# Kernel tuning notes

Measured on AMD Instinct MI355X. Metric: run time of the kernel, lower is better.

The kernel has to match this reference:

```python
import jax, jax.numpy as jnp
import numpy as np
import math

NUM_HEAD = 8
QK_DIM = 32       # in_dim // num_head
V_DIM = 32
KV_STRIDE = 2
Q_STRIDE = 1
LOCAL_RANGE = 16  # hard_range
POS_DIM = 256     # position_embedding_dim (= in_dim)
POS_MAG = 1.0
WAVE = 1000.0


def _position_feats(h, w, h_kv, w_kv, fcx_w, fcy_w):
    # sinusoidal embedding of (query_pos - key_pos), then linear projection per head
    fr = jnp.arange(POS_DIM // 4, dtype=jnp.float32)
    dim_mat = WAVE ** (4.0 / POS_DIM * fr)                 # (POS_DIM/4,)

    def emb(n_q, n_kv):
        diff = (jnp.arange(n_q, dtype=jnp.float32)[:, None] * Q_STRIDE
                - jnp.arange(n_kv, dtype=jnp.float32)[None, :] * KV_STRIDE) * POS_MAG
        a = diff[:, :, None] / dim_mat                      # (n_q, n_kv, POS_DIM/4)
        return jnp.concatenate([jnp.sin(a), jnp.cos(a)], axis=2)  # (n_q, n_kv, POS_DIM/2)

    inv_sqrt2 = 1.0 / math.sqrt(2.0)
    pfx = jnp.einsum('wkf,of->wko', emb(w, w_kv), fcx_w)
    pfx = pfx.reshape(w, w_kv, NUM_HEAD, QK_DIM).transpose(2, 0, 1, 3) * inv_sqrt2  # (H,w,w_kv,d)
    pfy = jnp.einsum('ykf,of->yko', emb(h, h_kv), fcy_w)
    pfy = pfy.reshape(h, h_kv, NUM_HEAD, QK_DIM).transpose(2, 0, 1, 3) * inv_sqrt2  # (H,h,h_kv,d)
    return pfx, pfy


def _local_mask(h, w, h_kv, w_kv):
    # True where attention is FORBIDDEN (matches masked_fill_ semantics of the map)
    R, s = LOCAL_RANGE, KV_STRIDE

    def axis_keep(n_q, n_kv):
        i = jnp.arange(n_q)
        k = jnp.arange(n_kv)
        lo = jnp.maximum((i - R) // s, 0)
        hi = (i + R + 1) // s + 1
        return (k[None, :] >= lo[:, None]) & (k[None, :] < hi[:, None])  # (n_q, n_kv)

    keep_y = axis_keep(h, h_kv)
    keep_x = axis_keep(w, w_kv)
    keep = keep_y[:, None, :, None] & keep_x[None, :, None, :]  # (h,w,h_kv,w_kv)
    return ~keep


def reference(x_input, q_w, k_w, v_w, fcx_w, fcy_w, appr_bias, geom_bias,
              proj_w, proj_b, gamma):
    n, c, h, w = x_input.shape
    H, d = NUM_HEAD, QK_DIM
    x_q = x_input                                   # q_stride == 1
    x_kv = x_input[:, :, ::KV_STRIDE, ::KV_STRIDE]  # AvgPool(kernel=1, stride=2)
    h_kv, w_kv = x_kv.shape[2], x_kv.shape[3]

    # 1x1 conv projections
    q = jnp.einsum('nchw,oc->nohw', x_q, q_w).reshape(n, H, d, h, w).transpose(0, 1, 3, 4, 2)  # (n,H,h,w,d)
    k = jnp.einsum('nchw,oc->nohw', x_kv, k_w).reshape(n, H, d, h_kv * w_kv)                   # (n,H,d,K)
    v = jnp.einsum('nchw,oc->nohw', x_kv, v_w).reshape(n, H, V_DIM, h_kv * w_kv).transpose(0, 1, 3, 2)  # (n,H,K,v)

    pfx, pfy = _position_feats(h, w, h_kv, w_kv, fcx_w, fcy_w)
    ab = appr_bias.reshape(1, H, 1, 1, d)
    gb = geom_bias.reshape(1, H, 1, 1, d)

    # appr-appr + bias-appr:  (q + appr_bias) @ k
    energy = jnp.einsum('nhyxd,nhdk->nhyxk', q + ab, k).reshape(n, H, h, w, h_kv, w_kv)
    # appr-position + bias-position, separable over x and y
    qg = q + gb
    energy = energy + jnp.einsum('nhyxd,hxkd->nhyxk', qg, pfx)[:, :, :, :, None, :]
    energy = energy + jnp.einsum('nhyxd,hykd->nhyxk', qg, pfy)[:, :, :, :, :, None]

    mask = _local_mask(h, w, h_kv, w_kv)  # (h,w,h_kv,w_kv), True = masked
    energy = jnp.where(mask[None, None], -jnp.inf, energy)
    energy = energy.reshape(n, H, h * w, h_kv * w_kv)

    attn = jax.nn.softmax(energy, axis=3)
    out = jnp.einsum('nhqk,nhkv->nhqv', attn, v)               # (n,H,h*w,v)
    out = out.transpose(0, 1, 3, 2).reshape(n, H * V_DIM, h, w)
    out = jnp.einsum('nchw,oc->nohw', out, proj_w) + proj_b[None, :, None, None]
    return gamma.reshape(()) * out + x_input


def setup_inputs() -> dict:
    key = jax.random.key(0)
    ks = jax.random.split(key, 11)
    s = 0.05  # keep attention logits in a sane range
    return {
        'x_input': jax.random.normal(ks[0], (2, 256, 64, 64), jnp.float32),
        'q_w': jax.random.normal(ks[1], (256, 256), jnp.float32) * s,
        'k_w': jax.random.normal(ks[2], (256, 256), jnp.float32) * s,
        'v_w': jax.random.normal(ks[3], (256, 256), jnp.float32) * s,
        'fcx_w': jax.random.normal(ks[4], (256, 128), jnp.float32) * s,
        'fcy_w': jax.random.normal(ks[5], (256, 128), jnp.float32) * s,
        'appr_bias': jax.random.normal(ks[6], (256,), jnp.float32) * s,
        'geom_bias': jax.random.normal(ks[7], (256,), jnp.float32) * s,
        'proj_w': jax.random.normal(ks[8], (256, 256), jnp.float32) * s,
        'proj_b': jax.random.normal(ks[9], (256,), jnp.float32) * s,
        'gamma': jax.random.normal(ks[10], (1,), jnp.float32),
    }
```

## Files before the change

### kernel.cpp

```cpp
#include <hip/hip_runtime.h>
#include <hip/hip_bf16.h>
#include <math.h>

#define NB   2
#define CC   256
#define PQ   4096
#define PKV  1024

#define NF (-INFINITY)
#define M0 24.0f
#define EXSTRIDE 36
#define EYSTRIDE 20

typedef __attribute__((ext_vector_type(8))) short short8;
typedef __attribute__((ext_vector_type(4))) float f32x4;

__global__ __launch_bounds__(256) void prep_kernel(
    const float* __restrict__ q_w, const float* __restrict__ k_w,
    const float* __restrict__ v_w, const float* __restrict__ proj_w,
    __hip_bfloat16* __restrict__ qw_b, __hip_bfloat16* __restrict__ kw_b,
    __hip_bfloat16* __restrict__ vw_b, __hip_bfloat16* __restrict__ pw_b,
    const float* __restrict__ fcx, const float* __restrict__ fcy,
    __hip_bfloat16* __restrict__ pembx_b, __hip_bfloat16* __restrict__ pemby_b,
    const float* __restrict__ x, __hip_bfloat16* __restrict__ xb) {
  __shared__ __align__(16) float shbuf[64 * 65];
  const int bid = blockIdx.x;
  const int tid = threadIdx.x;
  if (bid < 256) {
    const int which = bid >> 6;
    const float* src = (which == 0) ? q_w : (which == 1) ? k_w
                       : (which == 2) ? v_w : proj_w;
    __hip_bfloat16* dst = (which == 0) ? qw_b : (which == 1) ? kw_b
                          : (which == 2) ? vw_b : pw_b;
    const int i = (bid & 63) * 256 + tid;
    const float4 v = reinterpret_cast<const float4*>(src)[i];
    short4 s;
    s.x = __builtin_bit_cast(short, __float2bfloat16(v.x));
    s.y = __builtin_bit_cast(short, __float2bfloat16(v.y));
    s.z = __builtin_bit_cast(short, __float2bfloat16(v.z));
    s.w = __builtin_bit_cast(short, __float2bfloat16(v.w));
    reinterpret_cast<short4*>(dst)[i] = s;
  } else if (bid < 508) {
    float* feat = shbuf;
    const int pb = bid - 256;
    const int dd = pb >> 1;
    const int which = pb & 1;
    const float* FC = which ? fcy : fcx;
    __hip_bfloat16* OUT = which ? pemby_b : pembx_b;
    if (tid < 64) {
      const float diff = (float)(dd - 62);
      const float dm = powf(1000.f, (float)tid * (1.f / 64.f));
      const float aa = diff / dm;
      feat[tid] = sinf(aa);
      feat[tid + 64] = cosf(aa);
    }
    __syncthreads();
    const float4* row4 = reinterpret_cast<const float4*>(FC + tid * 128);
    const float4* f4 = reinterpret_cast<const float4*>(feat);
    float s0 = 0.f, s1 = 0.f, s2 = 0.f, s3 = 0.f;
#pragma unroll
    for (int f = 0; f < 32; ++f) {
      const float4 fv = f4[f];
      const float4 rv = row4[f];
      s0 = fmaf(fv.x, rv.x, s0);
      s1 = fmaf(fv.y, rv.y, s1);
      s2 = fmaf(fv.z, rv.z, s2);
      s3 = fmaf(fv.w, rv.w, s3);
    }
    const float s = ((s0 + s1) + (s2 + s3)) * 0.70710678118654752440f;
    OUT[(size_t)dd * 256 + tid] = __float2bfloat16(s);
  } else {
    float (*t)[65] = reinterpret_cast<float(*)[65]>(shbuf);
    const int b = bid - 508;
    const int p0 = (b & 63) * 64;
    const int c0 = ((b >> 6) & 3) * 64;
    const int n = b >> 8;
    {
      const int pl = tid & 63, cg = tid >> 6;
#pragma unroll
      for (int i = 0; i < 16; ++i) {
        const int cl = cg * 16 + i;
        t[cl][pl] = x[((size_t)n * 256 + c0 + cl) * PQ + p0 + pl];
      }
    }
    __syncthreads();
    const int cl = tid & 63;
#pragma unroll
    for (int j = 0; j < 16; ++j) {
      const int pl = (tid >> 6) + 4 * j;
      ((__hip_bfloat16*)xb)[((size_t)n * PQ + p0 + pl) * 256 + c0 + cl] =
          __float2bfloat16(t[cl][pl]);
    }
  }
}

__global__ __launch_bounds__(256) void gemm_qkv_kernel(
    const __hip_bfloat16* __restrict__ xb,
    const __hip_bfloat16* __restrict__ qw, const __hip_bfloat16* __restrict__ kw,
    const __hip_bfloat16* __restrict__ vw, const float* __restrict__ ab,
    const float* __restrict__ gb, __hip_bfloat16* __restrict__ qab,
    __hip_bfloat16* __restrict__ qgb, __hip_bfloat16* __restrict__ k_lb,
    __hip_bfloat16* __restrict__ v_t) {
  const int bid = blockIdx.x;
  const int tid = threadIdx.x;
  const int wv = tid >> 6, l = tid & 63, lc = l & 15, lq = l >> 4;
  if (bid < 1024) {
    const int n = bid & 1;
    const int o0 = ((bid >> 1) & 3) * 64;
    const int p0 = (bid >> 3) * 32;
    const short* ar =
        (const short*)qw + ((size_t)(o0 + wv * 16 + lc)) * 256 + 8 * lq;
    const short* bbase =
        (const short*)xb + ((size_t)n * PQ + p0) * 256 + 8 * lq;
    const short* b0p = bbase + (size_t)(0 + lc) * 256;
    const short* b1p = bbase + (size_t)(16 + lc) * 256;
    f32x4 acc0 = {0.f, 0.f, 0.f, 0.f};
    f32x4 acc1 = {0.f, 0.f, 0.f, 0.f};
#pragma unroll
    for (int kt = 0; kt < 8; ++kt) {
      const short8 af = *reinterpret_cast<const short8*>(ar + kt * 32);
      acc0 = __builtin_amdgcn_mfma_f32_16x16x32_bf16(
          af, *reinterpret_cast<const short8*>(b0p + kt * 32), acc0, 0, 0, 0);
      acc1 = __builtin_amdgcn_mfma_f32_16x16x32_bf16(
          af, *reinterpret_cast<const short8*>(b1p + kt * 32), acc1, 0, 0, 0);
    }
#pragma unroll
    for (int r = 0; r < 4; ++r) {
      const int o = o0 + wv * 16 + 4 * lq + r;
      const float abo = ab[o], gbo = gb[o];
      const int head = o >> 5, dd = o & 31;
      const size_t gbase = (size_t)(n * 8 + head) * PQ;
      const float a_[2] = {acc0[r], acc1[r]};
#pragma unroll
      for (int nf = 0; nf < 2; ++nf) {
        const int p = p0 + 16 * nf + lc;
        const size_t idx = (gbase + p) * 32 + dd;
        qab[idx] = __float2bfloat16(a_[nf] + abo);
        qgb[idx] = __float2bfloat16(a_[nf] + gbo);
      }
    }
  } else {
    const int kb2 = bid - 1024;
    const int n = kb2 & 1;
    const int o0 = ((kb2 >> 1) & 3) * 64;
    const bool isV = ((kb2 >> 3) & 1) != 0;
    const int p0 = (kb2 >> 4) * 32;
    const __hip_bfloat16* W = isV ? vw : kw;
    const short* ar =
        (const short*)W + ((size_t)(o0 + wv * 16 + lc)) * 256 + 8 * lq;
    const short* bb = (const short*)xb + (size_t)n * PQ * 256 + 8 * lq;
    const int pk0 = p0 + 0 + lc, pk1 = p0 + 16 + lc;
    const short* b0p = bb + (size_t)((pk0 >> 5) * 128 + (pk0 & 31) * 2) * 256;
    const short* b1p = bb + (size_t)((pk1 >> 5) * 128 + (pk1 & 31) * 2) * 256;
    f32x4 acc0 = {0.f, 0.f, 0.f, 0.f};
    f32x4 acc1 = {0.f, 0.f, 0.f, 0.f};
#pragma unroll
    for (int kt = 0; kt < 8; ++kt) {
      const short8 af = *reinterpret_cast<const short8*>(ar + kt * 32);
      acc0 = __builtin_amdgcn_mfma_f32_16x16x32_bf16(
          af, *reinterpret_cast<const short8*>(b0p + kt * 32), acc0, 0, 0, 0);
      acc1 = __builtin_amdgcn_mfma_f32_16x16x32_bf16(
          af, *reinterpret_cast<const short8*>(b1p + kt * 32), acc1, 0, 0, 0);
    }
#pragma unroll
    for (int r = 0; r < 4; ++r) {
      const int o = o0 + wv * 16 + 4 * lq + r;
      const int head = o >> 5, dd = o & 31;
      const float a_[2] = {acc0[r], acc1[r]};
#pragma unroll
      for (int nf = 0; nf < 2; ++nf) {
        const int p = p0 + 16 * nf + lc;
        if (!isV) {
          k_lb[((size_t)(n * 8 + head) * PKV + p) * 32 + dd] =
              __float2bfloat16(a_[nf]);
        } else {
          v_t[((size_t)(n * 8 + head) * 32 + dd) * PKV + p] =
              __float2bfloat16(a_[nf]);
        }
      }
    }
  }
}

__global__ __launch_bounds__(256) void exy_kernel(
    const __hip_bfloat16* __restrict__ qgb_b,
    const __hip_bfloat16* __restrict__ pembx_b,
    const __hip_bfloat16* __restrict__ pemby_b, float* __restrict__ EX,
    float* __restrict__ EY) {
  const int MODE = blockIdx.z;
  const int i = blockIdx.x;
  const int g = blockIdx.y;
  const int head = g & 7;
  const __hip_bfloat16* pemb_b = MODE ? pemby_b : pembx_b;
  const int wv = threadIdx.x >> 6;
  const int l = threadIdx.x & 63;
  const int lc = l & 15, lq = l >> 4;

  const int rowi = wv * 16 + lc;
  const int p = (MODE == 0) ? rowi * 64 + i : i * 64 + rowi;
  const short8 a = *reinterpret_cast<const short8*>(
      (const short*)qgb_b + ((size_t)g * PQ + p) * 32 + 8 * lq);

  int drow0, drow1;
  if (MODE == 0) {
    drow0 = i - 2 * lc + 62;
    drow1 = i - 2 * (lc + 16) + 62;
  } else {
    const int lo_y = max((i - 16) >> 1, 0);
    drow0 = i - 2 * (lo_y + lc) + 62;
    drow1 = i - 2 * (lo_y + lc + 16) + 62;
  }
  const short8 b0 = *reinterpret_cast<const short8*>(
      (const short*)pemb_b + (size_t)drow0 * 256 + head * 32 + 8 * lq);
  const short8 b1 = *reinterpret_cast<const short8*>(
      (const short*)pemb_b + (size_t)drow1 * 256 + head * 32 + 8 * lq);

  const f32x4 zero = {0.f, 0.f, 0.f, 0.f};
  const f32x4 c0 = __builtin_amdgcn_mfma_f32_16x16x32_bf16(a, b0, zero, 0, 0, 0);
  const f32x4 c1 = __builtin_amdgcn_mfma_f32_16x16x32_bf16(a, b1, zero, 0, 0, 0);

#pragma unroll
  for (int r = 0; r < 4; ++r) {
    const int rowr = wv * 16 + 4 * lq + r;
    const int pr = (MODE == 0) ? rowr * 64 + i : i * 64 + rowr;
    if (MODE == 0) {
      const int lox = max((i - 16) >> 1, 0);
      const int hix = min(((i + 17) >> 1) + 1, 32);
      float* o = EX + ((size_t)g * PQ + pr) * EXSTRIDE;
      o[lc] = (lc >= lox && lc < hix) ? (c0[r] - M0) : -1e30f;
      o[16 + lc] = (lc + 16 >= lox && lc + 16 < hix) ? (c1[r] - M0) : -1e30f;
      if (lc < 4) o[32 + lc] = -1e30f;
    } else {
      float* o = EY + ((size_t)g * PQ + pr) * EYSTRIDE;
      o[lc] = c0[r];
      if (lc < 4) o[16 + lc] = c1[r];
    }
  }
}

__global__ __launch_bounds__(512, 8) void attn_mfma_kernel(
    const __hip_bfloat16* __restrict__ qab_b,
    const __hip_bfloat16* __restrict__ k_lb,
    const __hip_bfloat16* __restrict__ v_t, const float* __restrict__ EX,
    const float* __restrict__ EY, __hip_bfloat16* __restrict__ attb) {
  const int g = blockIdx.y;
  const int nImg = g >> 3, hd = g & 7;
  const int bx = blockIdx.x & 3;
  const int by = blockIdx.x >> 2;
  const int tx = bx * 16;
  const int wv = threadIdx.x >> 6;
  const int yw = wv & 3;
  const int s = wv >> 2;
  const int y = by * 4 + yw;
  const int l = threadIdx.x & 63;
  const int lc = l & 15;
  const int lq = l >> 4;

  __shared__ float eybuf[4][EYSTRIDE][16];
  __shared__ float mrg[4][64][9];
  __shared__ float obuf[4][16][33];

  const int KLO = max((tx - 16) >> 1, 0);
  const int lo_y = max((y - 16) >> 1, 0);
  const int hi_y = min(((y + 17) >> 1) + 1, 32);
  const int NKY = hi_y - lo_y;

  const int xq = tx + lc;
  const int pq_ = y * 64 + xq;

  const short8 qa = *reinterpret_cast<const short8*>(
      (const short*)qab_b + ((size_t)g * PQ + pq_) * 32 + 8 * lq);

  const float* exr = EX + ((size_t)g * PQ + pq_) * EXSTRIDE;
  float exC0[4], exC1[4];
#pragma unroll
  for (int r = 0; r < 4; ++r) {
    exC0[r] = exr[KLO + 4 * lq + r];
    exC1[r] = exr[min(KLO + 16 + 4 * lq + r, 35)];
  }

  if (wv < 4) {
    const float* eyr = EY + ((size_t)g * PQ + pq_) * EYSTRIDE;
    const float4 e4 = *reinterpret_cast<const float4*>(eyr + 4 * lq);
#pragma unroll
    for (int j = 0; j < 4; ++j) eybuf[yw][4 * lq + j][lc] = e4[j];
    if (lq == 0) {
      const float4 e4b = *reinterpret_cast<const float4*>(eyr + 16);
#pragma unroll
      for (int j = 0; j < 4; ++j) eybuf[yw][16 + j][lc] = e4b[j];
    }
  }
  __syncthreads();

  const __hip_bfloat16* kb =
      k_lb + ((size_t)g * PKV + (size_t)lo_y * 32) * 32;
  const __hip_bfloat16* kb0 = kb + (KLO + lc) * 32 + 8 * lq;
  const __hip_bfloat16* kb1 = kb + min(KLO + 16 + lc, 31) * 32 + 8 * lq;
  const __hip_bfloat16* vb0 =
      v_t + ((size_t)g * 32 + lc) * PKV + (size_t)lo_y * 32 + KLO + 8 * lq;
  const __hip_bfloat16* vb1 = vb0 + 16 * PKV;

  f32x4 acc0 = {0.f, 0.f, 0.f, 0.f};
  f32x4 acc1 = {0.f, 0.f, 0.f, 0.f};
  float lp = 0.f;
  const int srcA = lc + ((l & 16) << 1);
  const int srcB = srcA + 16;
  const bool hiL = (l & 32) != 0;

#pragma unroll 1
  for (int t = s; t < NKY; t += 2) {
    const short8 k0 = *reinterpret_cast<const short8*>(kb0 + t * 1024);
    const short8 k1 = *reinterpret_cast<const short8*>(kb1 + t * 1024);
    const short8 v0 = *reinterpret_cast<const short8*>(vb0 + t * 32);
    const short8 v1 = *reinterpret_cast<const short8*>(vb1 + t * 32);
    const f32x4 zero = {0.f, 0.f, 0.f, 0.f};
    const f32x4 s0 = __builtin_amdgcn_mfma_f32_16x16x32_bf16(k0, qa, zero, 0, 0, 0);
    const f32x4 s1 = __builtin_amdgcn_mfma_f32_16x16x32_bf16(k1, qa, zero, 0, 0, 0);
    const float eyC = eybuf[yw][t][lc];
    float p0[4], p1[4];
#pragma unroll
    for (int r = 0; r < 4; ++r) {
      p0[r] = __expf(s0[r] + exC0[r] + eyC);
      p1[r] = __expf(s1[r] + exC1[r] + eyC);
    }
    lp += ((p0[0] + p0[1]) + (p0[2] + p0[3])) +
          ((p1[0] + p1[1]) + (p1[2] + p1[3]));
    int w00, w01, w10, w11;
    asm("v_cvt_pk_bf16_f32 %0, %1, %2" : "=v"(w00) : "v"(p0[0]), "v"(p0[1]));
    asm("v_cvt_pk_bf16_f32 %0, %1, %2" : "=v"(w01) : "v"(p0[2]), "v"(p0[3]));
    asm("v_cvt_pk_bf16_f32 %0, %1, %2" : "=v"(w10) : "v"(p1[0]), "v"(p1[1]));
    asm("v_cvt_pk_bf16_f32 %0, %1, %2" : "=v"(w11) : "v"(p1[2]), "v"(p1[3]));
    const int a0 = __shfl(w00, srcA, 64), b0 = __shfl(w10, srcA, 64);
    const int a1 = __shfl(w01, srcA, 64), b1 = __shfl(w11, srcA, 64);
    const int a2 = __shfl(w00, srcB, 64), b2 = __shfl(w10, srcB, 64);
    const int a3 = __shfl(w01, srcB, 64), b3 = __shfl(w11, srcB, 64);
    int4 pw;
    pw.x = hiL ? b0 : a0;
    pw.y = hiL ? b1 : a1;
    pw.z = hiL ? b2 : a2;
    pw.w = hiL ? b3 : a3;
    const short8 pf = __builtin_bit_cast(short8, pw);
    acc0 = __builtin_amdgcn_mfma_f32_16x16x32_bf16(pf, v0, acc0, 0, 0, 0);
    acc1 = __builtin_amdgcn_mfma_f32_16x16x32_bf16(pf, v1, acc1, 0, 0, 0);
  }

  if (s == 1) {
    float* m = mrg[yw][l];
#pragma unroll
    for (int r = 0; r < 4; ++r) m[r] = acc0[r];
#pragma unroll
    for (int r = 0; r < 4; ++r) m[4 + r] = acc1[r];
    m[8] = lp;
  }
  __syncthreads();
  if (s == 1) return;
  {
    const float* m = mrg[yw][l];
#pragma unroll
    for (int r = 0; r < 4; ++r) acc0[r] += m[r];
#pragma unroll
    for (int r = 0; r < 4; ++r) acc1[r] += m[4 + r];
    lp += m[8];
  }

  lp += __shfl_xor(lp, 16);
  lp += __shfl_xor(lp, 32);
  const float invall = 1.f / lp;

#pragma unroll
  for (int r = 0; r < 4; ++r) {
    const float inv = __shfl(invall, 4 * lq + r, 16);
    obuf[yw][4 * lq + r][lc] = acc0[r] * inv;
    obuf[yw][4 * lq + r][16 + lc] = acc1[r] * inv;
  }
  const int qp = l >> 2;
  const int ch = (l & 3) * 8;
  short8 sv;
#pragma unroll
  for (int j = 0; j < 8; ++j)
    sv[j] = __builtin_bit_cast(short, __float2bfloat16(obuf[yw][qp][ch + j]));
  const int p = y * 64 + tx + qp;
  *reinterpret_cast<short8*>(
      (short*)attb + ((size_t)nImg * PQ + p) * 256 + hd * 32 + ch) = sv;
}

__global__ __launch_bounds__(256) void gemm_out_kernel(
    const __hip_bfloat16* __restrict__ attb,
    const __hip_bfloat16* __restrict__ pw, const float* __restrict__ pb,
    const float* __restrict__ gamma, const float* __restrict__ x_in,
    float* __restrict__ out) {
  const int p0 = blockIdx.x * 32;
  const int o0 = blockIdx.y * 64;
  const int n = blockIdx.z;
  const int tid = threadIdx.x;
  const int wv = tid >> 6, l = tid & 63, lc = l & 15, lq = l >> 4;
  const short* ar =
      (const short*)pw + ((size_t)(o0 + wv * 16 + lc)) * 256 + 8 * lq;
  const short* bbase = (const short*)attb + ((size_t)n * PQ + p0) * 256 + 8 * lq;
  const short* b0p = bbase + (size_t)(0 + lc) * 256;
  const short* b1p = bbase + (size_t)(16 + lc) * 256;
  f32x4 acc0 = {0.f, 0.f, 0.f, 0.f};
  f32x4 acc1 = {0.f, 0.f, 0.f, 0.f};
#pragma unroll
  for (int kt = 0; kt < 8; ++kt) {
    const short8 af = *reinterpret_cast<const short8*>(ar + kt * 32);
    acc0 = __builtin_amdgcn_mfma_f32_16x16x32_bf16(
        af, *reinterpret_cast<const short8*>(b0p + kt * 32), acc0, 0, 0, 0);
    acc1 = __builtin_amdgcn_mfma_f32_16x16x32_bf16(
        af, *reinterpret_cast<const short8*>(b1p + kt * 32), acc1, 0, 0, 0);
  }
  const float gm = gamma[0];
#pragma unroll
  for (int r = 0; r < 4; ++r) {
    const int o = o0 + wv * 16 + 4 * lq + r;
    const float bo = pb[o];
    const size_t obase = ((size_t)n * 256 + o) * PQ;
    const size_t i0 = obase + (p0 + 0 + lc);
    const size_t i1 = obase + (p0 + 16 + lc);
    out[i0] = fmaf(gm, acc0[r] + bo, x_in[i0]);
    out[i1] = fmaf(gm, acc1[r] + bo, x_in[i1]);
  }
}

extern "C" void kernel_launch(void* const* d_in, const int* in_sizes, int n_in,
                              void* d_out, int out_size, void* d_ws,
                              size_t ws_size, hipStream_t stream) {
  const float* x = (const float*)d_in[0];
  const float* q_w = (const float*)d_in[1];
  const float* k_w = (const float*)d_in[2];
  const float* v_w = (const float*)d_in[3];
  const float* fcx_w = (const float*)d_in[4];
  const float* fcy_w = (const float*)d_in[5];
  const float* ab = (const float*)d_in[6];
  const float* gb = (const float*)d_in[7];
  const float* proj_w = (const float*)d_in[8];
  const float* proj_b = (const float*)d_in[9];
  const float* gamma = (const float*)d_in[10];
  float* out = (float*)d_out;

  float* ws = (float*)d_ws;
  float* EX = ws;
  float* EY = EX + 2359296;
  __hip_bfloat16* bp = (__hip_bfloat16*)(EY + 1310720);
  __hip_bfloat16* qab_b = bp;   bp += 2097152;
  __hip_bfloat16* qgb_b = bp;   bp += 2097152;
  __hip_bfloat16* k_lb = bp;    bp += 524288;
  __hip_bfloat16* v_t = bp;     bp += 524288;
  __hip_bfloat16* pembx_b = bp; bp += 32256;
  __hip_bfloat16* pemby_b = bp; bp += 32256;
  __hip_bfloat16* qw_b = bp;    bp += 65536;
  __hip_bfloat16* kw_b = bp;    bp += 65536;
  __hip_bfloat16* vw_b = bp;    bp += 65536;
  __hip_bfloat16* pw_b = bp;    bp += 65536;
  __hip_bfloat16* xb = bp;      bp += 2097152;
  __hip_bfloat16* attb = bp;    bp += 2097152;

  prep_kernel<<<dim3(1020), 256, 0, stream>>>(q_w, k_w, v_w, proj_w, qw_b,
                                              kw_b, vw_b, pw_b, fcx_w, fcy_w,
                                              pembx_b, pemby_b, x, xb);
  gemm_qkv_kernel<<<dim3(1536), 256, 0, stream>>>(xb, qw_b, kw_b, vw_b, ab,
                                                  gb, qab_b, qgb_b, k_lb, v_t);
  exy_kernel<<<dim3(64, 16, 2), 256, 0, stream>>>(qgb_b, pembx_b, pemby_b, EX,
                                                  EY);
  attn_mfma_kernel<<<dim3(64, 16), 512, 0, stream>>>(qab_b, k_lb, v_t, EX, EY,
                                                     attb);
  gemm_out_kernel<<<dim3(128, 4, 2), 256, 0, stream>>>(attb, pw_b, proj_b,
                                                       gamma, x, out);
}
```

Measured before the change: 88.71 us.

## Fuse Y-geometry logits into attention kernel and store X logits in bf16

```diff
diff --git a/kernel.cpp b/kernel.cpp
--- a/kernel.cpp
+++ b/kernel.cpp
@@ -182,67 +182,56 @@
   }
 }
 
-__global__ __launch_bounds__(256) void exy_kernel(
+__global__ __launch_bounds__(256) void ex_kernel(
     const __hip_bfloat16* __restrict__ qgb_b,
     const __hip_bfloat16* __restrict__ pembx_b,
-    const __hip_bfloat16* __restrict__ pemby_b, float* __restrict__ EX,
-    float* __restrict__ EY) {
-  const int MODE = blockIdx.z;
+    __hip_bfloat16* __restrict__ EX) {
   const int i = blockIdx.x;
   const int g = blockIdx.y;
   const int head = g & 7;
-  const __hip_bfloat16* pemb_b = MODE ? pemby_b : pembx_b;
   const int wv = threadIdx.x >> 6;
   const int l = threadIdx.x & 63;
   const int lc = l & 15, lq = l >> 4;
 
   const int rowi = wv * 16 + lc;
-  const int p = (MODE == 0) ? rowi * 64 + i : i * 64 + rowi;
+  const int p = rowi * 64 + i;
   const short8 a = *reinterpret_cast<const short8*>(
       (const short*)qgb_b + ((size_t)g * PQ + p) * 32 + 8 * lq);
 
-  int drow0, drow1;
-  if (MODE == 0) {
-    drow0 = i - 2 * lc + 62;
-    drow1 = i - 2 * (lc + 16) + 62;
-  } else {
-    const int lo_y = max((i - 16) >> 1, 0);
-    drow0 = i - 2 * (lo_y + lc) + 62;
-    drow1 = i - 2 * (lo_y + lc + 16) + 62;
-  }
+  const int drow0 = i - 2 * lc + 62;
+  const int drow1 = i - 2 * (lc + 16) + 62;
   const short8 b0 = *reinterpret_cast<const short8*>(
-      (const short*)pemb_b + (size_t)drow0 * 256 + head * 32 + 8 * lq);
+      (const short*)pembx_b + (size_t)drow0 * 256 + head * 32 + 8 * lq);
   const short8 b1 = *reinterpret_cast<const short8*>(
-      (const short*)pemb_b + (size_t)drow1 * 256 + head * 32 + 8 * lq);
+      (const short*)pembx_b + (size_t)drow1 * 256 + head * 32 + 8 * lq);
 
   const f32x4 zero = {0.f, 0.f, 0.f, 0.f};
   const f32x4 c0 = __builtin_amdgcn_mfma_f32_16x16x32_bf16(a, b0, zero, 0, 0, 0);
   const f32x4 c1 = __builtin_amdgcn_mfma_f32_16x16x32_bf16(a, b1, zero, 0, 0, 0);
 
+  const int lox = max((i - 16) >> 1, 0);
+  const int hix = min(((i + 17) >> 1) + 1, 32);
 #pragma unroll
   for (int r = 0; r < 4; ++r) {
     const int rowr = wv * 16 + 4 * lq + r;
-    const int pr = (MODE == 0) ? rowr * 64 + i : i * 64 + rowr;
-    if (MODE == 0) {
-      const int lox = max((i - 16) >> 1, 0);
-      const int hix = min(((i + 17) >> 1) + 1, 32);
-      float* o = EX + ((size_t)g * PQ + pr) * EXSTRIDE;
-      o[lc] = (lc >= lox && lc < hix) ? (c0[r] - M0) : -1e30f;
-      o[16 + lc] = (lc + 16 >= lox && lc + 16 < hix) ? (c1[r] - M0) : -1e30f;
-      if (lc < 4) o[32 + lc] = -1e30f;
-    } else {
-      float* o = EY + ((size_t)g * PQ + pr) * EYSTRIDE;
-      o[lc] = c0[r];
-      if (lc < 4) o[16 + lc] = c1[r];
-    }
+    const int pr = rowr * 64 + i;
+    __hip_bfloat16* o = EX + ((size_t)g * PQ + pr) * EXSTRIDE;
+    o[lc] = __float2bfloat16(
+        (lc >= lox && lc < hix) ? (c0[r] - M0) : -1e30f);
+    o[16 + lc] = __float2bfloat16(
+        (lc + 16 >= lox && lc + 16 < hix) ? (c1[r] - M0) : -1e30f);
+    if (lc < 4) o[32 + lc] = __float2bfloat16(-1e30f);
   }
 }
 
 __global__ __launch_bounds__(512, 8) void attn_mfma_kernel(
     const __hip_bfloat16* __restrict__ qab_b,
+    const __hip_bfloat16* __restrict__ qgb_b,
     const __hip_bfloat16* __restrict__ k_lb,
-    const __hip_bfloat16* __restrict__ v_t, const float* __restrict__ EX,
-    const float* __restrict__ EY, __hip_bfloat16* __restrict__ attb) {
+    const __hip_bfloat16* __restrict__ v_t,
+    const __hip_bfloat16* __restrict__ EX,
+    const __hip_bfloat16* __restrict__ pemby_b,
+    __hip_bfloat16* __restrict__ attb) {
   const int g = blockIdx.y;
   const int nImg = g >> 3, hd = g & 7;
   const int bx = blockIdx.x & 3;
@@ -271,23 +260,33 @@
   const short8 qa = *reinterpret_cast<const short8*>(
       (const short*)qab_b + ((size_t)g * PQ + pq_) * 32 + 8 * lq);
 
-  const float* exr = EX + ((size_t)g * PQ + pq_) * EXSTRIDE;
+  const short* exr = (const short*)EX + ((size_t)g * PQ + pq_) * EXSTRIDE;
   float exC0[4], exC1[4];
 #pragma unroll
   for (int r = 0; r < 4; ++r) {
-    exC0[r] = exr[KLO + 4 * lq + r];
-    exC1[r] = exr[min(KLO + 16 + 4 * lq + r, 35)];
-  }
-
-  if (wv < 4) {
-    const float* eyr = EY + ((size_t)g * PQ + pq_) * EYSTRIDE;
-    const float4 e4 = *reinterpret_cast<const float4*>(eyr + 4 * lq);
-#pragma unroll
-    for (int j = 0; j < 4; ++j) eybuf[yw][4 * lq + j][lc] = e4[j];
-    if (lq == 0) {
-      const float4 e4b = *reinterpret_cast<const float4*>(eyr + 16);
-#pragma unroll
-      for (int j = 0; j < 4; ++j) eybuf[yw][16 + j][lc] = e4b[j];
+    exC0[r] = __bfloat162float(
+        __builtin_bit_cast(__hip_bfloat16, exr[KLO + 4 * lq + r]));
+    exC1[r] = __bfloat162float(
+        __builtin_bit_cast(__hip_bfloat16, exr[min(KLO + 16 + 4 * lq + r, 35)]));
+  }
+
+  if (s == 0) {
+    const short8 ag = *reinterpret_cast<const short8*>(
+        (const short*)qgb_b + ((size_t)g * PQ + pq_) * 32 + 8 * lq);
+    const int dr0 = y - 2 * (lo_y + lc) + 62;
+    const int dr1 = y - 2 * (lo_y + lc + 16) + 62;
+    const short8 pb0 = *reinterpret_cast<const short8*>(
+        (const short*)pemby_b + (size_t)dr0 * 256 + hd * 32 + 8 * lq);
+    const short8 pb1 = *reinterpret_cast<const short8*>(
+        (const short*)pemby_b + (size_t)dr1 * 256 + hd * 32 + 8 * lq);
+    const f32x4 zero = {0.f, 0.f, 0.f, 0.f};
+    const f32x4 e0 = __builtin_amdgcn_mfma_f32_16x16x32_bf16(ag, pb0, zero, 0, 0, 0);
+    const f32x4 e1 = __builtin_amdgcn_mfma_f32_16x16x32_bf16(ag, pb1, zero, 0, 0, 0);
+#pragma unroll
+    for (int r = 0; r < 4; ++r) eybuf[yw][lc][4 * lq + r] = e0[r];
+    if (lc < 4) {
+#pragma unroll
+      for (int r = 0; r < 4; ++r) eybuf[yw][16 + lc][4 * lq + r] = e1[r];
     }
   }
   __syncthreads();
@@ -438,10 +437,8 @@
   const float* gamma = (const float*)d_in[10];
   float* out = (float*)d_out;
 
-  float* ws = (float*)d_ws;
-  float* EX = ws;
-  float* EY = EX + 2359296;
-  __hip_bfloat16* bp = (__hip_bfloat16*)(EY + 1310720);
+  __hip_bfloat16* bp = (__hip_bfloat16*)d_ws;
+  __hip_bfloat16* EX = bp;      bp += 2359296;
   __hip_bfloat16* qab_b = bp;   bp += 2097152;
   __hip_bfloat16* qgb_b = bp;   bp += 2097152;
   __hip_bfloat16* k_lb = bp;    bp += 524288;
@@ -460,10 +457,9 @@
                                               pembx_b, pemby_b, x, xb);
   gemm_qkv_kernel<<<dim3(1536), 256, 0, stream>>>(xb, qw_b, kw_b, vw_b, ab,
                                                   gb, qab_b, qgb_b, k_lb, v_t);
-  exy_kernel<<<dim3(64, 16, 2), 256, 0, stream>>>(qgb_b, pembx_b, pemby_b, EX,
-                                                  EY);
-  attn_mfma_kernel<<<dim3(64, 16), 512, 0, stream>>>(qab_b, k_lb, v_t, EX, EY,
-                                                     attb);
+  ex_kernel<<<dim3(64, 16), 256, 0, stream>>>(qgb_b, pembx_b, EX);
+  attn_mfma_kernel<<<dim3(64, 16), 512, 0, stream>>>(qab_b, qgb_b, k_lb, v_t,
+                                                     EX, pemby_b, attb);
   gemm_out_kernel<<<dim3(128, 4, 2), 256, 0, stream>>>(attb, pw_b, proj_b,
                                                        gamma, x, out);
 }
```

After: 86.05 us. 1.03x faster.
